# Kernel tuning notes

Hardware: AMD Instinct MI355X
Metric: run time of the kernel (lower is better)

The kernel has to match this reference:

```python
import jax, jax.numpy as jnp
import numpy as np

BS, C_IN, N_TF, D_MODEL, N_HEADS, D_FF, D_COMP = 32, 32, 128, 512, 8, 2048, 8
D_K = D_MODEL // N_HEADS
SCALE = D_K ** (-0.5)
EPS = 1e-5


def _ln(x, g, b):
    m = x.mean(-1, keepdims=True)
    v = ((x - m) ** 2).mean(-1, keepdims=True)
    return (x - m) / jnp.sqrt(v + EPS) * g + b


def setup_inputs() -> dict:
    key = jax.random.key(0)
    ks = jax.random.split(key, 16)
    dm, da, dff = D_MODEL, D_K * N_HEADS, D_FF
    s = lambda k, shape, sc: jax.random.normal(k, shape, jnp.float32) * sc
    return {
        "src": s(ks[0], (BS * C_IN, N_TF, dm), 1.0),
        "Wq": s(ks[1], (da, dm), dm ** -0.5), "bq": jnp.zeros((da,), jnp.float32),
        "Wk": s(ks[2], (da, dm), dm ** -0.5), "bk": jnp.zeros((da,), jnp.float32),
        "Wv": s(ks[3], (da, dm), dm ** -0.5), "bv": jnp.zeros((da,), jnp.float32),
        "Wo": s(ks[4], (dm, da), da ** -0.5), "bo": jnp.zeros((dm,), jnp.float32),
        "router": s(ks[5], (1, N_HEADS, D_COMP, D_K), 1.0),
        "m_expand": s(ks[6], (1, C_IN, D_COMP), 1.0),
        "pos_embd": jnp.zeros((1, D_COMP, da), jnp.float32),
        "g1": jnp.ones((dm,), jnp.float32), "b1": jnp.zeros((dm,), jnp.float32),
        "Wf1": s(ks[7], (dff, dm), dm ** -0.5), "bf1": jnp.zeros((dff,), jnp.float32),
        "Wf2": s(ks[8], (dm, dff), dff ** -0.5), "bf2": jnp.zeros((dm,), jnp.float32),
        "g2": jnp.ones((dm,), jnp.float32), "b2": jnp.zeros((dm,), jnp.float32),
    }


def reference(src, Wq, bq, Wk, bk, Wv, bv, Wo, bo, router, m_expand, pos_embd,
              g1, b1, Wf1, bf1, Wf2, bf2, g2, b2):
    B, h, dk, dm = BS * C_IN, N_HEADS, D_K, D_MODEL
    da = h * dk
    # projections -> [B, h, n_tf, d_k]
    q = (src @ Wq.T + bq).reshape(B, N_TF, h, dk).transpose(0, 2, 1, 3)
    k = (src @ Wk.T + bk).reshape(B, N_TF, h, dk).transpose(0, 2, 1, 3)
    v = (src @ Wv.T + bv).reshape(B, N_TF, h, dk).transpose(0, 2, 1, 3)
    # temporal attention
    scores = jnp.einsum('bhqd,bhkd->bhqk', q, k) * SCALE
    attn = jax.nn.softmax(scores, axis=-1)
    out_tf = jnp.einsum('bhqk,bhkd->bhqd', attn, v)  # [B,h,n_tf,d_k]
    out_tf = out_tf.transpose(0, 2, 1, 3).reshape(B, N_TF, da)
    # channel compression path (b_tf_2_bs=False)
    # keys: [B,h,d_k,n_tf] -> [bs,h,d_k,c_in*n_tf] (channel-major flatten, as in torch)
    kc = k.transpose(0, 1, 3, 2).reshape(BS, C_IN, h, dk, N_TF)
    kc = kc.transpose(0, 2, 3, 1, 4).reshape(BS, h, dk, C_IN * N_TF)
    # values: [bs,h,n_tf*c_in,d_k] (time-major flatten, as in torch)
    vc = v.reshape(BS, C_IN, h, N_TF, dk)
    vc = vc.transpose(0, 2, 3, 1, 4).reshape(BS, h, N_TF * C_IN, dk)
    qc = jnp.broadcast_to(router, (BS, h, D_COMP, dk))
    sc = jnp.einsum('bhqd,bhdk->bhqk', qc, kc) * SCALE
    ac = jax.nn.softmax(sc, axis=-1)
    oc = jnp.einsum('bhqk,bhkd->bhqd', ac, vc)  # [bs,h,d_comp,d_k]
    oc = oc.transpose(0, 2, 1, 3).reshape(BS, D_COMP, da) + pos_embd[0]
    chan = jnp.einsum('cq,bqd->bcd', m_expand[0], oc)  # [bs,c_in,da]
    chan = chan.reshape(B, 1, da)
    merged = out_tf + chan
    attn_out = merged @ Wo.T + bo
    x = _ln(src + attn_out, g1, b1)
    ff = jax.nn.gelu(x @ Wf1.T + bf1, approximate=False) @ Wf2.T + bf2
    x = _ln(x + ff, g2, b2)
    return x
```

## Files before the change

### kernel.cpp

```cpp
#include <hip/hip_runtime.h>
#include <math.h>

typedef unsigned short u16;
typedef unsigned int u32;
typedef __attribute__((ext_vector_type(8))) short bf16x8;
typedef __attribute__((ext_vector_type(4))) float f32x4;

__device__ __forceinline__ float bf2f(u16 u) {
    union { u32 i; float f; } x; x.i = ((u32)u) << 16; return x.f;
}
__device__ __forceinline__ u16 f2bf(float f) {
    union { float f; u32 i; } x; x.f = f;
    u32 i = x.i;
    return (u16)((i + 0x7FFFu + ((i >> 16) & 1u)) >> 16);
}
__device__ __forceinline__ void async_copy16(void* lds, const void* g) {
    __builtin_amdgcn_global_load_lds(
        (const __attribute__((address_space(1))) void*)g,
        (__attribute__((address_space(3))) void*)lds, 16, 0, 0);
}

__global__ __launch_bounds__(256) void conv_kernel(
    const float* __restrict__ in, u16* __restrict__ out)
{
    const int i = (blockIdx.x * 256 + threadIdx.x) * 4;
    float4 v = *(const float4*)&in[i];
    u32 lo = (u32)f2bf(v.x) | ((u32)f2bf(v.y) << 16);
    u32 hi = (u32)f2bf(v.z) | ((u32)f2bf(v.w) << 16);
    *(uint2*)&out[i] = make_uint2(lo, hi);
}

__global__ __launch_bounds__(256) void pack_bias_kernel(
    const float* __restrict__ a, const float* __restrict__ b,
    const float* __restrict__ c, float* __restrict__ out)
{
    const int i = blockIdx.x * 256 + threadIdx.x;
    out[i] = i < 512 ? a[i] : (i < 1024 ? b[i - 512] : c[i - 1024]);
}

template<int ACT, int OBF, int RES, int NSPLIT>
__global__ __launch_bounds__(512) void gemm256_kernel(
    const u16* __restrict__ Ag, const u16* __restrict__ Bg,
    const float* __restrict__ bias, const void* __restrict__ resv,
    void* __restrict__ Ov, u16* __restrict__ O2, u16* __restrict__ O3,
    int M, int N, int K)
{
    __shared__ u16 As[2][16384];
    __shared__ u16 Bs[2][16384];
    const int tid = threadIdx.x;
    const int lane = tid & 63;
    const int wm = tid >> 8, wn = (tid >> 6) & 3;
    const int li = lane & 15, g = lane >> 4;

    const int nwg = gridDim.x;
    const int wg = ((blockIdx.x & 7) * (nwg >> 3)) + (blockIdx.x >> 3);
    const int ntn = N >> 8;
    const int m0 = (wg / ntn) << 8;
    const int n0 = (wg % ntn) << 8;

    f32x4 acc[8][4] = {};

    const int nk = K >> 6;
    {
        #pragma unroll
        for (int i = 0; i < 4; ++i) {
            const int base = i * 512 + (tid & 448);
            const int L = base + lane;
            const int row = L >> 3;
            const int cc = (L & 7) ^ (row & 7);
            async_copy16(&As[0][base * 8], &Ag[(size_t)(m0 + row) * K + cc * 8]);
            async_copy16(&Bs[0][base * 8], &Bg[(size_t)(n0 + row) * K + cc * 8]);
        }
    }
    __syncthreads();

    for (int t = 0; t < nk; ++t) {
        const int cur = t & 1;
        if (t + 1 < nk) {
            const int k0 = (t + 1) << 6;
            #pragma unroll
            for (int i = 0; i < 4; ++i) {
                const int base = i * 512 + (tid & 448);
                const int L = base + lane;
                const int row = L >> 3;
                const int cc = (L & 7) ^ (row & 7);
                async_copy16(&As[cur ^ 1][base * 8],
                             &Ag[(size_t)(m0 + row) * K + k0 + cc * 8]);
                async_copy16(&Bs[cur ^ 1][base * 8],
                             &Bg[(size_t)(n0 + row) * K + k0 + cc * 8]);
            }
        }
        #pragma unroll
        for (int ks = 0; ks < 2; ++ks) {
            bf16x8 af[8], bf_[4];
            #pragma unroll
            for (int mi = 0; mi < 8; ++mi) {
                const int row = wm * 128 + mi * 16 + li;
                const int ch = (ks * 4 + g) ^ (row & 7);
                af[mi] = *(const bf16x8*)&As[cur][row * 64 + ch * 8];
            }
            #pragma unroll
            for (int ni = 0; ni < 4; ++ni) {
                const int row = wn * 64 + ni * 16 + li;
                const int ch = (ks * 4 + g) ^ (row & 7);
                bf_[ni] = *(const bf16x8*)&Bs[cur][row * 64 + ch * 8];
            }
            #pragma unroll
            for (int mi = 0; mi < 8; ++mi)
                #pragma unroll
                for (int ni = 0; ni < 4; ++ni)
                    acc[mi][ni] = __builtin_amdgcn_mfma_f32_16x16x32_bf16(
                        af[mi], bf_[ni], acc[mi][ni], 0, 0, 0);
        }
        __syncthreads();
    }

    #pragma unroll
    for (int mi = 0; mi < 8; ++mi)
    #pragma unroll
    for (int ni = 0; ni < 4; ++ni) {
        const int colb = n0 + wn * 64 + ni * 16;
        #pragma unroll
        for (int r = 0; r < 4; ++r) {
            const int row = m0 + wm * 128 + mi * 16 + g * 4 + r;
            const int col = colb + li;
            float v = acc[mi][ni][r] + bias[col];
            if (RES == 1) v += ((const float*)resv)[(size_t)row * N + col];
            if (RES == 2) v += bf2f(((const u16*)resv)[(size_t)row * N + col]);
            if (ACT == 1) v = 0.5f * v * (1.0f + erff(v * 0.70710678118f));
            if (NSPLIT == 1) {
                const int sec = colb >> 9;
                u16* dst = sec == 0 ? (u16*)Ov : (sec == 1 ? O2 : O3);
                dst[(size_t)row * 512 + (col & 511)] = f2bf(v);
            } else if (OBF) {
                ((u16*)Ov)[(size_t)row * N + col] = f2bf(v);
            } else {
                ((float*)Ov)[(size_t)row * N + col] = v;
            }
        }
    }
}

__global__ __launch_bounds__(256) void attn_mfma_kernel(
    const u16* __restrict__ Q, const u16* __restrict__ K,
    const u16* __restrict__ V, const float* __restrict__ chan,
    u16* __restrict__ merged)
{
    __shared__ u16 pool[26112];
    u16* Ks = pool;
    u16* Ps = pool;
    u16* Vt = pool + 17408;
    const int b = blockIdx.x, h = blockIdx.y;
    const int tid = threadIdx.x, lane = tid & 63, w = tid >> 6;
    const int li = lane & 15, g = lane >> 4;
    const size_t gbase = (size_t)b * 128 * 512 + (size_t)h * 64;

    #pragma unroll
    for (int i = 0; i < 4; ++i) {
        const int c = tid + i * 256;
        const int t = c >> 3, dc = c & 7;
        bf16x8 kv = *(const bf16x8*)&K[gbase + (size_t)t * 512 + dc * 8];
        *(bf16x8*)&Ks[t * 72 + dc * 8] = kv;
        bf16x8 vv = *(const bf16x8*)&V[gbase + (size_t)t * 512 + dc * 8];
        #pragma unroll
        for (int j = 0; j < 8; ++j) Vt[(dc * 8 + j) * 136 + t] = (u16)vv[j];
    }
    bf16x8 qf[2][2];
    #pragma unroll
    for (int mi = 0; mi < 2; ++mi)
        #pragma unroll
        for (int ks = 0; ks < 2; ++ks)
            qf[mi][ks] = *(const bf16x8*)
                &Q[gbase + (size_t)(w * 32 + mi * 16 + li) * 512 + ks * 32 + g * 8];
    __syncthreads();

    f32x4 sacc[2][8] = {};
    #pragma unroll
    for (int nj = 0; nj < 8; ++nj) {
        bf16x8 kf0 = *(const bf16x8*)&Ks[(nj * 16 + li) * 72 + g * 8];
        bf16x8 kf1 = *(const bf16x8*)&Ks[(nj * 16 + li) * 72 + 32 + g * 8];
        #pragma unroll
        for (int mi = 0; mi < 2; ++mi) {
            sacc[mi][nj] = __builtin_amdgcn_mfma_f32_16x16x32_bf16(
                qf[mi][0], kf0, sacc[mi][nj], 0, 0, 0);
            sacc[mi][nj] = __builtin_amdgcn_mfma_f32_16x16x32_bf16(
                qf[mi][1], kf1, sacc[mi][nj], 0, 0, 0);
        }
    }
    float linv[2][4];
    #pragma unroll
    for (int mi = 0; mi < 2; ++mi)
    #pragma unroll
    for (int r = 0; r < 4; ++r) {
        float mx = -1e30f;
        #pragma unroll
        for (int nj = 0; nj < 8; ++nj) {
            sacc[mi][nj][r] *= 0.125f;
            mx = fmaxf(mx, sacc[mi][nj][r]);
        }
        mx = fmaxf(mx, __shfl_xor(mx, 1));
        mx = fmaxf(mx, __shfl_xor(mx, 2));
        mx = fmaxf(mx, __shfl_xor(mx, 4));
        mx = fmaxf(mx, __shfl_xor(mx, 8));
        float l = 0.f;
        #pragma unroll
        for (int nj = 0; nj < 8; ++nj) {
            float p = __expf(sacc[mi][nj][r] - mx);
            sacc[mi][nj][r] = p;
            l += p;
        }
        l += __shfl_xor(l, 1);
        l += __shfl_xor(l, 2);
        l += __shfl_xor(l, 4);
        l += __shfl_xor(l, 8);
        linv[mi][r] = 1.f / l;
    }
    __syncthreads();
    #pragma unroll
    for (int mi = 0; mi < 2; ++mi)
    #pragma unroll
    for (int r = 0; r < 4; ++r)
        #pragma unroll
        for (int nj = 0; nj < 8; ++nj)
            Ps[(w * 32 + mi * 16 + g * 4 + r) * 136 + nj * 16 + li] =
                f2bf(sacc[mi][nj][r]);
    __syncthreads();

    f32x4 oacc[2][4] = {};
    #pragma unroll
    for (int ks = 0; ks < 4; ++ks) {
        bf16x8 pf[2];
        #pragma unroll
        for (int mi = 0; mi < 2; ++mi)
            pf[mi] = *(const bf16x8*)&Ps[(w * 32 + mi * 16 + li) * 136 + ks * 32 + g * 8];
        #pragma unroll
        for (int ni = 0; ni < 4; ++ni) {
            bf16x8 vf = *(const bf16x8*)&Vt[(ni * 16 + li) * 136 + ks * 32 + g * 8];
            #pragma unroll
            for (int mi = 0; mi < 2; ++mi)
                oacc[mi][ni] = __builtin_amdgcn_mfma_f32_16x16x32_bf16(
                    pf[mi], vf, oacc[mi][ni], 0, 0, 0);
        }
    }
    #pragma unroll
    for (int mi = 0; mi < 2; ++mi)
    #pragma unroll
    for (int ni = 0; ni < 4; ++ni)
    #pragma unroll
    for (int r = 0; r < 4; ++r) {
        const int row = w * 32 + mi * 16 + g * 4 + r;
        const int col = ni * 16 + li;
        float v = oacc[mi][ni][r] * linv[mi][r] +
                  chan[(size_t)b * 512 + h * 64 + col];
        merged[gbase + (size_t)row * 512 + col] = f2bf(v);
    }
}

__global__ __launch_bounds__(1024) void chan_oc_kernel(
    const u16* __restrict__ K, const u16* __restrict__ V,
    const u16* __restrict__ router_bf, float* __restrict__ oc)
{
    __shared__ float S[8 * 4096];
    __shared__ float o_final[8 * 64];
    __shared__ float linv[8];
    const int bs = blockIdx.x, h = blockIdx.y;
    const int tid = threadIdx.x, lane = tid & 63, w = tid >> 6;
    const int li = lane & 15, g = lane >> 4;

    if (tid < 512) o_final[tid] = 0.f;

    bf16x8 af[2];
    #pragma unroll
    for (int ks = 0; ks < 2; ++ks) {
        bf16x8 t = {};
        if (li < 8) t = *(const bf16x8*)&router_bf[(h * 8 + li) * 64 + ks * 32 + g * 8];
        af[ks] = t;
    }
    #pragma unroll 4
    for (int n = w * 16; n < w * 16 + 16; ++n) {
        f32x4 acc = {};
        #pragma unroll
        for (int ks = 0; ks < 2; ++ks) {
            const int j = n * 16 + li;
            const int kc = j >> 7, kt = j & 127;
            bf16x8 bf_ = *(const bf16x8*)
                &K[((size_t)((bs * 32 + kc) * 128 + kt)) * 512 + h * 64 + ks * 32 + g * 8];
            acc = __builtin_amdgcn_mfma_f32_16x16x32_bf16(af[ks], bf_, acc, 0, 0, 0);
        }
        if (g < 2) {
            #pragma unroll
            for (int r = 0; r < 4; ++r)
                S[(g * 4 + r) * 4096 + n * 16 + li] = acc[r] * 0.125f;
        }
    }
    __syncthreads();
    if (w < 8) {
        float l = 0.f;
        #pragma unroll 8
        for (int i = 0; i < 64; ++i) {
            float p = __expf(S[w * 4096 + i * 64 + lane]);
            S[w * 4096 + i * 64 + lane] = p;
            l += p;
        }
        #pragma unroll
        for (int off = 1; off < 64; off <<= 1) l += __shfl_xor(l, off);
        if (lane == 0) linv[w] = 1.f / l;
    }
    __syncthreads();
    float o[8][4] = {};
    for (int it = 0; it < 64; ++it) {
        const int row = w * 256 + it * 4 + g;
        const int j = (row & 127) * 32 + (row >> 7);
        const uint2 vv = *(const uint2*)
            &V[((size_t)bs * 4096 + row) * 512 + h * 64 + li * 4];
        const float v0 = bf2f((u16)(vv.x & 0xffff)), v1 = bf2f((u16)(vv.x >> 16));
        const float v2 = bf2f((u16)(vv.y & 0xffff)), v3 = bf2f((u16)(vv.y >> 16));
        #pragma unroll
        for (int q = 0; q < 8; ++q) {
            const float p = S[q * 4096 + j];
            o[q][0] += p * v0; o[q][1] += p * v1;
            o[q][2] += p * v2; o[q][3] += p * v3;
        }
    }
    #pragma unroll
    for (int q = 0; q < 8; ++q)
        #pragma unroll
        for (int i = 0; i < 4; ++i) {
            float v = o[q][i];
            v += __shfl_xor(v, 16);
            v += __shfl_xor(v, 32);
            if (g == 0) atomicAdd(&o_final[q * 64 + li * 4 + i], v);
        }
    __syncthreads();
    if (tid < 512) {
        const int q = tid >> 6, d = tid & 63;
        oc[((size_t)bs * 8 + q) * 512 + h * 64 + d] = o_final[q * 64 + d] * linv[q];
    }
}

__global__ __launch_bounds__(512) void chan_combine_kernel(
    const float* __restrict__ oc, const float* __restrict__ pos,
    const float* __restrict__ mexp, float* __restrict__ chan)
{
    const int b = blockIdx.x;
    const int bs = b >> 5, c = b & 31;
    const int d = threadIdx.x;
    float acc = 0.f;
    #pragma unroll
    for (int q = 0; q < 8; ++q)
        acc += mexp[c * 8 + q] *
               (oc[((size_t)bs * 8 + q) * 512 + d] + pos[q * 512 + d]);
    chan[(size_t)b * 512 + d] = acc;
}

template<int IBF, int OBF>
__global__ __launch_bounds__(256) void ln_kernel(
    const void* __restrict__ inv, const float* __restrict__ g,
    const float* __restrict__ bb, void* __restrict__ out)
{
    const size_t row = (size_t)blockIdx.x * 4 + (threadIdx.x >> 6);
    const int t = threadIdx.x & 63;
    float4 v0, v1;
    if (IBF) {
        const u16* p = (const u16*)inv + row * 512;
        uint2 a = *(const uint2*)(p + t * 4);
        uint2 b = *(const uint2*)(p + 256 + t * 4);
        v0 = make_float4(bf2f((u16)(a.x & 0xffff)), bf2f((u16)(a.x >> 16)),
                         bf2f((u16)(a.y & 0xffff)), bf2f((u16)(a.y >> 16)));
        v1 = make_float4(bf2f((u16)(b.x & 0xffff)), bf2f((u16)(b.x >> 16)),
                         bf2f((u16)(b.y & 0xffff)), bf2f((u16)(b.y >> 16)));
    } else {
        const float* p = (const float*)inv + row * 512;
        v0 = *(const float4*)(p + t * 4);
        v1 = *(const float4*)(p + 256 + t * 4);
    }
    float s = (v0.x + v0.y) + (v0.z + v0.w) + (v1.x + v1.y) + (v1.z + v1.w);
    #pragma unroll
    for (int off = 1; off < 64; off <<= 1) s += __shfl_xor(s, off);
    const float mean = s * (1.0f / 512.0f);
    float a, ss = 0.f;
    a = v0.x - mean; ss += a * a;  a = v0.y - mean; ss += a * a;
    a = v0.z - mean; ss += a * a;  a = v0.w - mean; ss += a * a;
    a = v1.x - mean; ss += a * a;  a = v1.y - mean; ss += a * a;
    a = v1.z - mean; ss += a * a;  a = v1.w - mean; ss += a * a;
    #pragma unroll
    for (int off = 1; off < 64; off <<= 1) ss += __shfl_xor(ss, off);
    const float rstd = rsqrtf(ss * (1.0f / 512.0f) + 1e-5f);
    const int c0 = t * 4, c1 = 256 + t * 4;
    float4 g0 = *(const float4*)(g + c0), g1v = *(const float4*)(g + c1);
    float4 b0 = *(const float4*)(bb + c0), b1v = *(const float4*)(bb + c1);
    float r0 = (v0.x - mean) * rstd * g0.x + b0.x;
    float r1 = (v0.y - mean) * rstd * g0.y + b0.y;
    float r2 = (v0.z - mean) * rstd * g0.z + b0.z;
    float r3 = (v0.w - mean) * rstd * g0.w + b0.w;
    float r4 = (v1.x - mean) * rstd * g1v.x + b1v.x;
    float r5 = (v1.y - mean) * rstd * g1v.y + b1v.y;
    float r6 = (v1.z - mean) * rstd * g1v.z + b1v.z;
    float r7 = (v1.w - mean) * rstd * g1v.w + b1v.w;
    if (OBF) {
        u16* ob = (u16*)out + row * 512;
        uint2 u0, u1;
        u0.x = (u32)f2bf(r0) | ((u32)f2bf(r1) << 16);
        u0.y = (u32)f2bf(r2) | ((u32)f2bf(r3) << 16);
        u1.x = (u32)f2bf(r4) | ((u32)f2bf(r5) << 16);
        u1.y = (u32)f2bf(r6) | ((u32)f2bf(r7) << 16);
        *(uint2*)(ob + c0) = u0;
        *(uint2*)(ob + c1) = u1;
    } else {
        float* of = (float*)out + row * 512;
        *(float4*)(of + c0) = make_float4(r0, r1, r2, r3);
        *(float4*)(of + c1) = make_float4(r4, r5, r6, r7);
    }
}

extern "C" void kernel_launch(void* const* d_in, const int* in_sizes, int n_in,
                              void* d_out, int out_size, void* d_ws, size_t ws_size,
                              hipStream_t stream)
{
    const float* src    = (const float*)d_in[0];
    const float* Wq     = (const float*)d_in[1];
    const float* bq     = (const float*)d_in[2];
    const float* Wk     = (const float*)d_in[3];
    const float* bk     = (const float*)d_in[4];
    const float* Wv     = (const float*)d_in[5];
    const float* bv     = (const float*)d_in[6];
    const float* Wo     = (const float*)d_in[7];
    const float* bo     = (const float*)d_in[8];
    const float* router = (const float*)d_in[9];
    const float* mexp   = (const float*)d_in[10];
    const float* pos    = (const float*)d_in[11];
    const float* g1     = (const float*)d_in[12];
    const float* b1     = (const float*)d_in[13];
    const float* Wf1    = (const float*)d_in[14];
    const float* bf1    = (const float*)d_in[15];
    const float* Wf2    = (const float*)d_in[16];
    const float* bf2_   = (const float*)d_in[17];
    const float* g2     = (const float*)d_in[18];
    const float* b2     = (const float*)d_in[19];

    float* out = (float*)d_out;

    char* ws = (char*)d_ws;
    u16*   Qb     = (u16*)(ws + 0);
    u16*   Kb     = (u16*)(ws + 134217728);
    u16*   Vb     = (u16*)(ws + 268435456);
    u16*   merged = (u16*)(ws + 402653184);
    float* oc     = (float*)(ws + 536870912);
    float* chan   = (float*)(ws + 537395200);
    u16*   wob    = (u16*)(ws + 541065216);
    u16*   wf1b   = (u16*)(ws + 541589504);
    u16*   wf2b   = (u16*)(ws + 543686656);
    u16*   wqkvb  = (u16*)(ws + 545783808);
    float* qkvbias= (float*)(ws + 547356672);
    u16*   routbf = (u16*)(ws + 547362816);
    u16*   srcb   = (u16*)(ws + 402653184);
    u16*   h1b    = (u16*)(ws + 134217728);
    u16*   xb     = (u16*)(ws + 0);
    u16*   gbuf   = (u16*)(ws + 268435456);
    u16*   h2b    = (u16*)(ws + 402653184);

    const dim3 blk(256);
    const dim3 blk512(512);
    conv_kernel<<<dim3(65536), blk, 0, stream>>>(src, srcb);
    conv_kernel<<<dim3(256),  blk, 0, stream>>>(Wq,  wqkvb);
    conv_kernel<<<dim3(256),  blk, 0, stream>>>(Wk,  wqkvb + 262144);
    conv_kernel<<<dim3(256),  blk, 0, stream>>>(Wv,  wqkvb + 524288);
    conv_kernel<<<dim3(256),  blk, 0, stream>>>(Wo,  wob);
    conv_kernel<<<dim3(1024), blk, 0, stream>>>(Wf1, wf1b);
    conv_kernel<<<dim3(1024), blk, 0, stream>>>(Wf2, wf2b);
    conv_kernel<<<dim3(4),    blk, 0, stream>>>(router, routbf);
    pack_bias_kernel<<<dim3(6), blk, 0, stream>>>(bq, bk, bv, qkvbias);
    gemm256_kernel<0, 1, 0, 1><<<dim3(3072), blk512, 0, stream>>>(
        srcb, wqkvb, qkvbias, nullptr, Qb, Kb, Vb, 131072, 1536, 512);
    chan_oc_kernel<<<dim3(32, 8), dim3(1024), 0, stream>>>(Kb, Vb, routbf, oc);
    chan_combine_kernel<<<dim3(1024), dim3(512), 0, stream>>>(oc, pos, mexp, chan);
    attn_mfma_kernel<<<dim3(1024, 8), blk, 0, stream>>>(Qb, Kb, Vb, chan, merged);
    gemm256_kernel<0, 1, 1, 0><<<dim3(1024), blk512, 0, stream>>>(
        merged, wob, bo, src, h1b, nullptr, nullptr, 131072, 512, 512);
    ln_kernel<1, 1><<<dim3(32768), blk, 0, stream>>>(h1b, g1, b1, xb);
    for (int c = 0; c < 4; ++c) {
        const size_t off = (size_t)c * 32768 * 512;
        const size_t off2k = (size_t)c * 32768 * 2048;
        gemm256_kernel<1, 1, 0, 0><<<dim3(1024), blk512, 0, stream>>>(
            xb + off, wf1b, bf1, nullptr, gbuf, nullptr, nullptr,
            32768, 2048, 512);
        gemm256_kernel<0, 1, 2, 0><<<dim3(256), blk512, 0, stream>>>(
            gbuf, wf2b, bf2_, xb + off, h2b + off, nullptr, nullptr,
            32768, 512, 2048);
    }
    ln_kernel<1, 0><<<dim3(32768), blk, 0, stream>>>(h2b, g2, b2, out);
}
```

Before: 1.814 ms.

## Restructure GEMM mainloop into half-K stages with interleaved async loads

The GEMM main loop now splits each 64-wide K tile into two 32-wide LDS sub-buffers. It replaces the full __syncthreads with vmcnt waits plus raw barriers and issues the next tile's A and B loads between MFMA groups, raising priority around the MFMA bursts. The aim is to overlap global-to-LDS copies with compute and to cut barrier stalls. Separately, the FFN is processed in two chunks of 65536 rows instead of four, with h2b moved to a different workspace slot, to reduce launches and improve occupancy per launch. This adds fragile manual wait-count synchronisation and a larger gbuf footprint.

```diff
diff --git a/kernel.cpp b/kernel.cpp
--- a/kernel.cpp
+++ b/kernel.cpp
@@ -45,8 +45,8 @@
     void* __restrict__ Ov, u16* __restrict__ O2, u16* __restrict__ O3,
     int M, int N, int K)
 {
-    __shared__ u16 As[2][16384];
-    __shared__ u16 Bs[2][16384];
+    __shared__ u16 As[2][2][8192];
+    __shared__ u16 Bs[2][2][8192];
     const int tid = threadIdx.x;
     const int lane = tid & 63;
     const int wm = tid >> 8, wn = (tid >> 6) & 3;
@@ -58,62 +58,113 @@
     const int m0 = (wg / ntn) << 8;
     const int n0 = (wg % ntn) << 8;
 
+    const u16 *sa0, *sa1, *sb0, *sb1;
+    int wb0, wb1;
+    {
+        int L = tid, p = L >> 3, q = L & 7, u = q ^ (p & 7);
+        int row = 2 * p + (u >> 2), c = u & 3;
+        wb0 = (tid & 448) * 8 + ((tid & 63) << 3);
+        sa0 = Ag + (size_t)(m0 + row) * K + c * 8;
+        sb0 = Bg + (size_t)(n0 + row) * K + c * 8;
+        L = 512 + tid; p = L >> 3; q = L & 7; u = q ^ (p & 7);
+        row = 2 * p + (u >> 2); c = u & 3;
+        sa1 = Ag + (size_t)(m0 + row) * K + c * 8;
+        sb1 = Bg + (size_t)(n0 + row) * K + c * 8;
+    }
+    const int db0 = (tid & 448) * 8;
+    const int db1 = (512 + (tid & 448)) * 8;
+
+    int offA[8], offB[4];
+    #pragma unroll
+    for (int i = 0; i < 8; ++i) {
+        const int row = wm * 128 + i * 16 + li;
+        const int p = row >> 1;
+        offA[i] = (p * 8 + ((((row & 1) << 2) | g) ^ (p & 7))) * 8;
+    }
+    #pragma unroll
+    for (int i = 0; i < 4; ++i) {
+        const int row = wn * 64 + i * 16 + li;
+        const int p = row >> 1;
+        offB[i] = (p * 8 + ((((row & 1) << 2) | g) ^ (p & 7))) * 8;
+    }
+
     f32x4 acc[8][4] = {};
-
     const int nk = K >> 6;
-    {
-        #pragma unroll
-        for (int i = 0; i < 4; ++i) {
-            const int base = i * 512 + (tid & 448);
-            const int L = base + lane;
-            const int row = L >> 3;
-            const int cc = (L & 7) ^ (row & 7);
-            async_copy16(&As[0][base * 8], &Ag[(size_t)(m0 + row) * K + cc * 8]);
-            async_copy16(&Bs[0][base * 8], &Bg[(size_t)(n0 + row) * K + cc * 8]);
-        }
-    }
-    __syncthreads();
+
+#define STAGE_A(buf, ks, kc) do { \
+    async_copy16(&As[buf][ks][db0], sa0 + (kc)); \
+    async_copy16(&As[buf][ks][db1], sa1 + (kc)); } while (0)
+#define STAGE_B(buf, ks, kc) do { \
+    async_copy16(&Bs[buf][ks][db0], sb0 + (kc)); \
+    async_copy16(&Bs[buf][ks][db1], sb1 + (kc)); } while (0)
+
+    STAGE_A(0, 0, 0); STAGE_B(0, 0, 0);
+    STAGE_A(0, 1, 32); STAGE_B(0, 1, 32);
 
     for (int t = 0; t < nk; ++t) {
-        const int cur = t & 1;
-        if (t + 1 < nk) {
-            const int k0 = (t + 1) << 6;
+        const int cur = t & 1, nxt = cur ^ 1;
+        const int kn = (t + 1 < nk ? t + 1 : t) << 6;
+        bf16x8 af[4], bfr[4];
+
+        asm volatile("s_waitcnt vmcnt(4)" ::: "memory");
+        __builtin_amdgcn_s_barrier();
+        STAGE_A(nxt, 0, kn);
+        #pragma unroll
+        for (int i = 0; i < 4; ++i) af[i]  = *(const bf16x8*)&As[cur][0][offA[i]];
+        #pragma unroll
+        for (int i = 0; i < 4; ++i) bfr[i] = *(const bf16x8*)&Bs[cur][0][offB[i]];
+        __builtin_amdgcn_s_setprio(1);
+        #pragma unroll
+        for (int mi = 0; mi < 4; ++mi)
             #pragma unroll
-            for (int i = 0; i < 4; ++i) {
-                const int base = i * 512 + (tid & 448);
-                const int L = base + lane;
-                const int row = L >> 3;
-                const int cc = (L & 7) ^ (row & 7);
-                async_copy16(&As[cur ^ 1][base * 8],
-                             &Ag[(size_t)(m0 + row) * K + k0 + cc * 8]);
-                async_copy16(&Bs[cur ^ 1][base * 8],
-                             &Bg[(size_t)(n0 + row) * K + k0 + cc * 8]);
-            }
-        }
-        #pragma unroll
-        for (int ks = 0; ks < 2; ++ks) {
-            bf16x8 af[8], bf_[4];
+            for (int ni = 0; ni < 4; ++ni)
+                acc[mi][ni] = __builtin_amdgcn_mfma_f32_16x16x32_bf16(
+                    af[mi], bfr[ni], acc[mi][ni], 0, 0, 0);
+        __builtin_amdgcn_s_setprio(0);
+
+        STAGE_B(nxt, 0, kn);
+        #pragma unroll
+        for (int i = 0; i < 4; ++i) af[i] = *(const bf16x8*)&As[cur][0][offA[4 + i]];
+        __builtin_amdgcn_s_setprio(1);
+        #pragma unroll
+        for (int mi = 0; mi < 4; ++mi)
             #pragma unroll
-            for (int mi = 0; mi < 8; ++mi) {
-                const int row = wm * 128 + mi * 16 + li;
-                const int ch = (ks * 4 + g) ^ (row & 7);
-                af[mi] = *(const bf16x8*)&As[cur][row * 64 + ch * 8];
-            }
+            for (int ni = 0; ni < 4; ++ni)
+                acc[4 + mi][ni] = __builtin_amdgcn_mfma_f32_16x16x32_bf16(
+                    af[mi], bfr[ni], acc[4 + mi][ni], 0, 0, 0);
+        __builtin_amdgcn_s_setprio(0);
+
+        asm volatile("s_waitcnt vmcnt(4)" ::: "memory");
+        __builtin_amdgcn_s_barrier();
+        STAGE_A(nxt, 1, kn + 32);
+        #pragma unroll
+        for (int i = 0; i < 4; ++i) af[i]  = *(const bf16x8*)&As[cur][1][offA[i]];
+        #pragma unroll
+        for (int i = 0; i < 4; ++i) bfr[i] = *(const bf16x8*)&Bs[cur][1][offB[i]];
+        __builtin_amdgcn_s_setprio(1);
+        #pragma unroll
+        for (int mi = 0; mi < 4; ++mi)
             #pragma unroll
-            for (int ni = 0; ni < 4; ++ni) {
-                const int row = wn * 64 + ni * 16 + li;
-                const int ch = (ks * 4 + g) ^ (row & 7);
-                bf_[ni] = *(const bf16x8*)&Bs[cur][row * 64 + ch * 8];
-            }
+            for (int ni = 0; ni < 4; ++ni)
+                acc[mi][ni] = __builtin_amdgcn_mfma_f32_16x16x32_bf16(
+                    af[mi], bfr[ni], acc[mi][ni], 0, 0, 0);
+        __builtin_amdgcn_s_setprio(0);
+
+        STAGE_B(nxt, 1, kn + 32);
+        #pragma unroll
+        for (int i = 0; i < 4; ++i) af[i] = *(const bf16x8*)&As[cur][1][offA[4 + i]];
+        __builtin_amdgcn_s_setprio(1);
+        #pragma unroll
+        for (int mi = 0; mi < 4; ++mi)
             #pragma unroll
-            for (int mi = 0; mi < 8; ++mi)
-                #pragma unroll
-                for (int ni = 0; ni < 4; ++ni)
-                    acc[mi][ni] = __builtin_amdgcn_mfma_f32_16x16x32_bf16(
-                        af[mi], bf_[ni], acc[mi][ni], 0, 0, 0);
-        }
-        __syncthreads();
-    }
+            for (int ni = 0; ni < 4; ++ni)
+                acc[4 + mi][ni] = __builtin_amdgcn_mfma_f32_16x16x32_bf16(
+                    af[mi], bfr[ni], acc[4 + mi][ni], 0, 0, 0);
+        __builtin_amdgcn_s_setprio(0);
+    }
+    asm volatile("s_waitcnt vmcnt(0)" ::: "memory");
+#undef STAGE_A
+#undef STAGE_B
 
     #pragma unroll
     for (int mi = 0; mi < 8; ++mi)
@@ -457,7 +508,7 @@
     u16*   h1b    = (u16*)(ws + 134217728);
     u16*   xb     = (u16*)(ws + 0);
     u16*   gbuf   = (u16*)(ws + 268435456);
-    u16*   h2b    = (u16*)(ws + 402653184);
+    u16*   h2b    = (u16*)(ws + 134217728);
 
     const dim3 blk(256);
     const dim3 blk512(512);
@@ -478,15 +529,14 @@
     gemm256_kernel<0, 1, 1, 0><<<dim3(1024), blk512, 0, stream>>>(
         merged, wob, bo, src, h1b, nullptr, nullptr, 131072, 512, 512);
     ln_kernel<1, 1><<<dim3(32768), blk, 0, stream>>>(h1b, g1, b1, xb);
-    for (int c = 0; c < 4; ++c) {
-        const size_t off = (size_t)c * 32768 * 512;
-        const size_t off2k = (size_t)c * 32768 * 2048;
-        gemm256_kernel<1, 1, 0, 0><<<dim3(1024), blk512, 0, stream>>>(
+    for (int c = 0; c < 2; ++c) {
+        const size_t off = (size_t)c * 65536 * 512;
+        gemm256_kernel<1, 1, 0, 0><<<dim3(2048), blk512, 0, stream>>>(
             xb + off, wf1b, bf1, nullptr, gbuf, nullptr, nullptr,
-            32768, 2048, 512);
-        gemm256_kernel<0, 1, 2, 0><<<dim3(256), blk512, 0, stream>>>(
+            65536, 2048, 512);
+        gemm256_kernel<0, 1, 2, 0><<<dim3(512), blk512, 0, stream>>>(
             gbuf, wf2b, bf2_, xb + off, h2b + off, nullptr, nullptr,
-            32768, 512, 2048);
+            65536, 512, 2048);
     }
     ln_kernel<1, 0><<<dim3(32768), blk, 0, stream>>>(h2b, g2, b2, out);
 }
```

Measured after the change: 1.814 ms (median of 2 runs). About the same (+0.0%).
